# Kernel optimization log

Measured on AMD Instinct MI355X. Metric: run time of the kernel, lower is better.

The kernel has to match this reference:

```python
import jax, jax.numpy as jnp
import numpy as np

EPS = 1e-5  # GraphNorm eps


def setup_inputs() -> dict:
    key = jax.random.key(0)
    ks = jax.random.split(key, 8)
    B, N, D, L = 8, 2048, 128, 3
    return {
        "instance": jax.random.uniform(ks[0], (B, N, 2), jnp.float32),
        "Wn": jax.random.normal(ks[1], (D, 2), jnp.float32) * 0.5,
        "bn": jnp.zeros((D,), jnp.float32),
        "Wg": jax.random.normal(ks[2], (L, D, D), jnp.float32) / np.sqrt(D).astype(np.float32),
        "bg": jnp.zeros((L, D), jnp.float32),
        "gn_w": jnp.ones((D,), jnp.float32),
        "gn_b": jnp.zeros((D,), jnp.float32),
        "gn_a": jnp.ones((D,), jnp.float32),
    }


def reference(instance, Wn, bn, Wg, bg, gn_w, gn_b, gn_a):
    # instance: [B, N, 2] city coordinates. Graph is complete, so the PyG
    # edge-list GCN over all (i != j) pairs + self-loops is exactly a dense
    # symmetric-normalized adjacency matmul per graph.
    B, N, _ = instance.shape
    # pairwise Euclidean distances (cdist), safe sqrt to keep diagonal exact 0
    sq = jnp.sum(instance * instance, axis=-1)                      # [B, N]
    d2 = sq[:, :, None] + sq[:, None, :] - 2.0 * jnp.einsum(
        'bnd,bmd->bnm', instance, instance)                          # [B, N, N]
    pos = d2 > 0
    dist = jnp.where(pos, jnp.sqrt(jnp.where(pos, d2, 1.0)), 0.0)    # [B, N, N]
    # GCN edge weights = distances, self-loops added with weight 1.0
    A = dist + jnp.eye(N, dtype=dist.dtype)
    deg = jnp.sum(A, axis=-1)                                        # [B, N]
    dinv = jax.lax.rsqrt(deg)
    An = dinv[:, :, None] * A * dinv[:, None, :]                     # D^-1/2 A D^-1/2

    h = jnp.einsum('bne,de->bnd', instance, Wn) + bn                 # proj_node
    for l in range(Wg.shape[0]):
        # GCNConv: aggregate normalized messages of lin(x), then bias
        hw = jnp.einsum('bnm,bmd->bnd', An, jnp.einsum('bnd,ed->bne', h, Wg[l])) + bg[l]
        h = jnp.tanh(hw) + h                                         # activation + residual
        # GraphNorm (shared params across layers): per-graph, per-feature stats
        mean = jnp.mean(h, axis=1, keepdims=True)                    # [B, 1, D]
        sub = h - gn_a * mean
        var = jnp.mean(sub * sub, axis=1, keepdims=True)
        h = gn_w * sub * jax.lax.rsqrt(var + EPS) + gn_b
    return h  # [B, N, D] (unbatch+stack of equal-size graphs)
```

## Files before the change

kernel.cpp:

```cpp
#include <hip/hip_runtime.h>
#include <hip/hip_bf16.h>
#include <math.h>

#define BB 8
#define NN 2048
#define DD 128
#define LL 3
#define GN_EPS 1e-5f

typedef __attribute__((ext_vector_type(8))) short bf16x8;
typedef __attribute__((ext_vector_type(4))) float f32x4;
typedef __attribute__((ext_vector_type(8))) unsigned short u16x8;

#define FSQRT(x) __builtin_amdgcn_sqrtf(x)

#define GLL16(gp, lp) __builtin_amdgcn_global_load_lds( \
    (const __attribute__((address_space(1))) void*)(gp), \
    (__attribute__((address_space(3))) void*)(lp), 16, 0, 0)

#define WAIT_VM10 0x0F7A

__device__ __forceinline__ unsigned short f2bf(float f) {
    union { float f; unsigned u; } v; v.f = f;
    return (unsigned short)((v.u + 0x8000u) >> 16);
}

__device__ __forceinline__ float fast_tanh(float x) {
    float e = __expf(-2.0f * fabsf(x));
    float t = (1.0f - e) * __builtin_amdgcn_rcpf(1.0f + e);
    return copysignf(t, x);
}

__device__ __forceinline__ void stats_sc(float ps, float pq, float a, float w_,
                                         float b_, float& s, float& c) {
    const float inv_n = 1.0f / (float)NN;
    float mean = ps * inv_n;
    float msq  = pq * inv_n;
    float var  = msq - mean * mean * a * (2.0f - a);
    float rstd = rsqrtf(var + GN_EPS);
    s = w_ * rstd;
    c = b_ - s * (a * mean);
}


__global__ __launch_bounds__(256)
void prep_wg(const float* __restrict__ Wg, unsigned short* __restrict__ wgf)
{
    const int f = blockIdx.x * 256 + threadIdx.x;
    const int l  = f >> 14;
    const int r  = f & 16383;
    const int dp = r >> 7;
    const int e  = r & 127;
    const int dpt = dp >> 4, ll = dp & 15;
    const int kc  = e >> 5,  eo = e & 31;
    wgf[((((l * 8 + dpt) * 4 + kc) * 16 + ll) << 5) + eo] = f2bf(Wg[f]);
}

__global__ __launch_bounds__(256)
void gen_pack(const float* __restrict__ inst, const float* __restrict__ Wn,
              const float* __restrict__ bn, unsigned short* __restrict__ Ap,
              float* __restrict__ dinv, float* __restrict__ h,
              float* __restrict__ psum, float* __restrict__ psq)
{
    __shared__ float cs[NN * 2];
    __shared__ float part[4][16];
    const int b     = blockIdx.x & 7;
    const int ntile = blockIdx.x >> 3;
    const int n0    = ntile * 16;
    const int tid   = threadIdx.x;
    const int w     = tid >> 6;
    const int lane  = tid & 63;
    const int lq    = lane >> 4;
    const int ll    = lane & 15;

    const float* instb = inst + b * NN * 2;
    for (int i = tid; i < (NN * 2) / 4; i += 256)
        ((float4*)cs)[i] = ((const float4*)instb)[i];
    __syncthreads();

    const int n = n0 + ll;
    const float nx = cs[n * 2 + 0];
    const float ny = cs[n * 2 + 1];

    u16x8* apw = (u16x8*)Ap + (size_t)(b * 128 + ntile) * 64 * 64 + (w * 16) * 64 + lane;

    const int diagkcg = ntile >> 1;
    float rs = 0.f;
    for (int kc = 0; kc < 16; ++kc) {
        const int kcg = w * 16 + kc;
        const int mb  = kcg * 32 + lq * 8;
        const float* cp = &cs[mb * 2];
        float4 c01 = *(const float4*)(cp + 0);
        float4 c23 = *(const float4*)(cp + 4);
        float4 c45 = *(const float4*)(cp + 8);
        float4 c67 = *(const float4*)(cp + 12);
        float mxx[8] = { c01.x, c01.z, c23.x, c23.z, c45.x, c45.z, c67.x, c67.z };
        float myy[8] = { c01.y, c01.w, c23.y, c23.w, c45.y, c45.w, c67.y, c67.w };
        float dist[8];
        #pragma unroll
        for (int j = 0; j < 8; ++j) {
            float dx = nx - mxx[j];
            float dy = ny - myy[j];
            dist[j] = FSQRT(dx * dx + dy * dy);
        }
        if (kcg == diagkcg) {
            #pragma unroll
            for (int j = 0; j < 8; ++j)
                if (mb + j == n) dist[j] = 1.0f;
        }
        u16x8 pk;
        #pragma unroll
        for (int j = 0; j < 8; ++j) {
            pk[j] = f2bf(dist[j]);
            rs += dist[j];
        }
        apw[kc * 64] = pk;
    }

    rs += __shfl_xor(rs, 16);
    rs += __shfl_xor(rs, 32);
    if (lq == 0) part[w][ll] = rs;
    __syncthreads();
    if (tid < 16)
        dinv[b * NN + n0 + tid] = rsqrtf(part[0][tid] + part[1][tid] +
                                         part[2][tid] + part[3][tid]);

    {
        const int d  = tid & 127;
        const int r0 = tid >> 7;
        const float w0 = Wn[d * 2 + 0];
        const float w1 = Wn[d * 2 + 1];
        const float bv = bn[d];
        #pragma unroll
        for (int r = r0; r < 16; r += 2) {
            const float x0 = cs[(n0 + r) * 2 + 0];
            const float x1 = cs[(n0 + r) * 2 + 1];
            h[((size_t)b * NN + n0 + r) * DD + d] = fmaf(x0, w0, fmaf(x1, w1, bv));
        }
    }
    if (blockIdx.x == 0) {
        for (int i = tid; i < LL * BB * DD; i += 256) { psum[i] = 0.f; psq[i] = 0.f; }
    }
}

template <bool HP>
__global__ __launch_bounds__(256)
void lin_mfma(const float* __restrict__ h, const unsigned short* __restrict__ wgf_l,
              const float* __restrict__ dinv,
              const float* __restrict__ psumP, const float* __restrict__ psqP,
              const float* __restrict__ ga, const float* __restrict__ gw,
              const float* __restrict__ gb, unsigned short* __restrict__ tp)
{
    __shared__ float sL[DD], cL[DD];
    const int tid  = threadIdx.x;
    const int b    = blockIdx.x & 7;
    const int tile = blockIdx.x >> 3;
    const int row0 = b * NN + tile * 32;
    const int w    = tid >> 6;
    const int lane = tid & 63;
    const int lq   = lane >> 4;
    const int ll   = lane & 15;

    if (tid < DD) {
        float s = 1.0f, c = 0.0f;
        if (HP)
            stats_sc(psumP[b * DD + tid], psqP[b * DD + tid],
                     ga[tid], gw[tid], gb[tid], s, c);
        sL[tid] = s; cL[tid] = c;
    }
    __syncthreads();

    bf16x8 aw[2][4];
    #pragma unroll
    for (int mt = 0; mt < 2; ++mt) {
        const int dpt = 2 * w + mt;
        #pragma unroll
        for (int kc = 0; kc < 4; ++kc)
            aw[mt][kc] = *(const bf16x8*)&wgf_l[(((dpt * 4 + kc) * 16 + ll) << 5) + lq * 8];
    }

    bf16x8 bh[2][4];
    #pragma unroll
    for (int nt = 0; nt < 2; ++nt) {
        const float* hrow = h + (size_t)(row0 + nt * 16 + ll) * DD;
        #pragma unroll
        for (int kc = 0; kc < 4; ++kc) {
            float4 h0 = *(const float4*)&hrow[kc * 32 + lq * 8];
            float4 h1 = *(const float4*)&hrow[kc * 32 + lq * 8 + 4];
            const int e0 = kc * 32 + lq * 8;
            bf16x8 p;
            p[0] = (short)f2bf(fmaf(sL[e0 + 0], h0.x, cL[e0 + 0]));
            p[1] = (short)f2bf(fmaf(sL[e0 + 1], h0.y, cL[e0 + 1]));
            p[2] = (short)f2bf(fmaf(sL[e0 + 2], h0.z, cL[e0 + 2]));
            p[3] = (short)f2bf(fmaf(sL[e0 + 3], h0.w, cL[e0 + 3]));
            p[4] = (short)f2bf(fmaf(sL[e0 + 4], h1.x, cL[e0 + 4]));
            p[5] = (short)f2bf(fmaf(sL[e0 + 5], h1.y, cL[e0 + 5]));
            p[6] = (short)f2bf(fmaf(sL[e0 + 6], h1.z, cL[e0 + 6]));
            p[7] = (short)f2bf(fmaf(sL[e0 + 7], h1.w, cL[e0 + 7]));
            bh[nt][kc] = p;
        }
    }

    f32x4 acc[2][2];
    #pragma unroll
    for (int i = 0; i < 2; ++i)
        #pragma unroll
        for (int j = 0; j < 2; ++j) acc[i][j] = (f32x4)0.0f;

    #pragma unroll
    for (int kc = 0; kc < 4; ++kc)
        #pragma unroll
        for (int nt = 0; nt < 2; ++nt)
            #pragma unroll
            for (int mt = 0; mt < 2; ++mt)
                acc[nt][mt] = __builtin_amdgcn_mfma_f32_16x16x32_bf16(
                    bh[nt][kc], aw[mt][kc], acc[nt][mt], 0, 0, 0);

    #pragma unroll
    for (int nt = 0; nt < 2; ++nt) {
        const int mloc0 = nt * 16 + lq * 4;
        const int lq_a  = mloc0 >> 3;
        const int j0    = mloc0 & 7;
        float4 di4 = *(const float4*)&dinv[row0 + mloc0];
        #pragma unroll
        for (int mt = 0; mt < 2; ++mt) {
            const int dt = 2 * w + mt;
            ushort4 pk;
            pk.x = f2bf(acc[nt][mt][0] * di4.x);
            pk.y = f2bf(acc[nt][mt][1] * di4.y);
            pk.z = f2bf(acc[nt][mt][2] * di4.z);
            pk.w = f2bf(acc[nt][mt][3] * di4.w);
            *(ushort4*)&tp[((size_t)((b * 64 + tile) * 8 + dt) * 64 + lq_a * 16 + ll) * 8 + j0] = pk;
        }
    }
}

template <bool HP>
__global__ __launch_bounds__(256, 3)
void agg_mfma(const unsigned short* __restrict__ Ap, const unsigned short* __restrict__ tp,
              const float* __restrict__ dinv, const float* __restrict__ bg_l,
              const float* __restrict__ psumP, const float* __restrict__ psqP,
              const float* __restrict__ ga, const float* __restrict__ gw,
              const float* __restrict__ gb,
              float* __restrict__ h, float* __restrict__ psum, float* __restrict__ psq)
{
    __shared__ char Abuf[7][4096];
    const int b     = blockIdx.x & 7;
    const int ntile = blockIdx.x >> 3;
    const int n0    = ntile * 16;
    const int tid   = threadIdx.x;
    const int w     = tid >> 6;
    const int lane  = tid & 63;
    const int lq    = lane >> 4;
    const int ll    = lane & 15;

    const unsigned short* apsrc = Ap + ((size_t)(b * 128 + ntile) * 64) * 512 + lane * 8;
    const unsigned short* tpb   = tp + ((size_t)b * 64 * 8) * 512 + lane * 8;

    f32x4 acc[2];
    acc[0] = (f32x4)0.0f;
    acc[1] = (f32x4)0.0f;

    bf16x8 fb[3][2][4];

#define GLLA(c) GLL16(apsrc + (size_t)((((c) & 15) * 4 + w)) * 512, \
                      &Abuf[(c) % 7][w * 1024]);
#define LOADB(c) { \
        const int kb_ = ((c) & 15) * 4; \
        _Pragma("unroll") \
        for (int s_ = 0; s_ < 4; ++s_) { \
            fb[(c) % 3][0][s_] = *(const bf16x8*)(tpb + (size_t)((kb_ + s_) * 8 + 2 * w + 0) * 512); \
            fb[(c) % 3][1][s_] = *(const bf16x8*)(tpb + (size_t)((kb_ + s_) * 8 + 2 * w + 1) * 512); \
        } \
    }

    GLLA(0) GLLA(1) GLLA(2) GLLA(3)
    LOADB(0)
    GLLA(4)
    LOADB(1)
    GLLA(5)

    #pragma unroll
    for (int k = 0; k < 16; ++k) {
        __builtin_amdgcn_s_waitcnt(WAIT_VM10);
        __builtin_amdgcn_s_barrier();
        __builtin_amdgcn_sched_barrier(0);
        bf16x8 af[4];
        const char* lb = &Abuf[k % 7][0];
        #pragma unroll
        for (int s = 0; s < 4; ++s)
            af[s] = *(const bf16x8*)(lb + s * 1024 + lane * 16);
        LOADB(k + 2)
        GLLA(k + 6)
        __builtin_amdgcn_sched_barrier(0);
        #pragma unroll
        for (int s = 0; s < 4; ++s) {
            acc[0] = __builtin_amdgcn_mfma_f32_16x16x32_bf16(fb[k % 3][0][s], af[s], acc[0], 0, 0, 0);
            acc[1] = __builtin_amdgcn_mfma_f32_16x16x32_bf16(fb[k % 3][1][s], af[s], acc[1], 0, 0, 0);
        }
    }
#undef GLLA
#undef LOADB

    const int n  = n0 + ll;
    const float di = dinv[b * NN + n];
    #pragma unroll
    for (int dtl = 0; dtl < 2; ++dtl) {
        const int d0 = (2 * w + dtl) * 16 + lq * 4;
        float4 bg4 = *(const float4*)&bg_l[d0];
        float sres[4] = {1.f, 1.f, 1.f, 1.f}, cres[4] = {0.f, 0.f, 0.f, 0.f};
        if (HP) {
            float4 ps4 = *(const float4*)&psumP[b * DD + d0];
            float4 pq4 = *(const float4*)&psqP[b * DD + d0];
            float4 ga4 = *(const float4*)&ga[d0];
            float4 gw4 = *(const float4*)&gw[d0];
            float4 gb4 = *(const float4*)&gb[d0];
            stats_sc(ps4.x, pq4.x, ga4.x, gw4.x, gb4.x, sres[0], cres[0]);
            stats_sc(ps4.y, pq4.y, ga4.y, gw4.y, gb4.y, sres[1], cres[1]);
            stats_sc(ps4.z, pq4.z, ga4.z, gw4.z, gb4.z, sres[2], cres[2]);
            stats_sc(ps4.w, pq4.w, ga4.w, gw4.w, gb4.w, sres[3], cres[3]);
        }
        size_t idx = ((size_t)b * NN + n) * DD + d0;
        float4 hv = *(const float4*)&h[idx];
        float outv[4];
        #pragma unroll
        for (int r = 0; r < 4; ++r) {
            float pre = di * acc[dtl][r] + (&bg4.x)[r];
            outv[r] = fast_tanh(pre) + fmaf(sres[r], (&hv.x)[r], cres[r]);
        }
        float4 ov = { outv[0], outv[1], outv[2], outv[3] };
        *(float4*)&h[idx] = ov;

        float hs[4], hq[4];
        #pragma unroll
        for (int r = 0; r < 4; ++r) { hs[r] = outv[r]; hq[r] = outv[r] * outv[r]; }
        #pragma unroll
        for (int off = 1; off < 16; off <<= 1) {
            #pragma unroll
            for (int r = 0; r < 4; ++r) {
                hs[r] += __shfl_xor(hs[r], off);
                hq[r] += __shfl_xor(hq[r], off);
            }
        }
        if (ll == 0) {
            #pragma unroll
            for (int r = 0; r < 4; ++r) {
                atomicAdd(&psum[b * DD + d0 + r], hs[r]);
                atomicAdd(&psq[b * DD + d0 + r], hq[r]);
            }
        }
    }
}

__global__ __launch_bounds__(256)
void apply_kernel(const float* __restrict__ h,
                  const float* __restrict__ psum2, const float* __restrict__ psq2,
                  const float* __restrict__ ga, const float* __restrict__ gw,
                  const float* __restrict__ gb, float* __restrict__ dst)
{
    const int i4 = blockIdx.x * 256 + threadIdx.x;
    const int dg = (i4 & 31) * 4;
    const int b  = i4 >> 16;
    float4 hv = ((const float4*)h)[i4];
    float o[4];
    #pragma unroll
    for (int j = 0; j < 4; ++j) {
        const int d = dg + j;
        float s, c;
        stats_sc(psum2[b * DD + d], psq2[b * DD + d], ga[d], gw[d], gb[d], s, c);
        o[j] = fmaf(s, (&hv.x)[j], c);
    }
    float4 ov = { o[0], o[1], o[2], o[3] };
    ((float4*)dst)[i4] = ov;
}

extern "C" void kernel_launch(void* const* d_in, const int* in_sizes, int n_in,
                              void* d_out, int out_size, void* d_ws, size_t ws_size,
                              hipStream_t stream)
{
    const float* inst = (const float*)d_in[0];
    const float* Wn   = (const float*)d_in[1];
    const float* bn   = (const float*)d_in[2];
    const float* Wg   = (const float*)d_in[3];
    const float* bg   = (const float*)d_in[4];
    const float* gw   = (const float*)d_in[5];
    const float* gb   = (const float*)d_in[6];
    const float* ga   = (const float*)d_in[7];
    float* out = (float*)d_out;

    float* ws   = (float*)d_ws;
    float* dinv = ws;
    float* h    = dinv + BB * NN;
    float* psum = h + (size_t)BB * NN * DD;
    float* psq  = psum + LL * BB * DD;
    unsigned short* wgf = (unsigned short*)(psq + LL * BB * DD);
    unsigned short* tp  = wgf + LL * DD * DD;
    unsigned short* Ap  = tp + (size_t)BB * DD * NN;

    prep_wg<<<(LL * DD * DD) / 256, 256, 0, stream>>>(Wg, wgf);
    gen_pack<<<1024, 256, 0, stream>>>(inst, Wn, bn, Ap, dinv, h, psum, psq);

    for (int l = 0; l < LL; ++l) {
        const unsigned short* wgl = wgf + (size_t)l * DD * DD;
        const float* psP = psum + (size_t)(l - 1) * BB * DD;
        const float* pqP = psq  + (size_t)(l - 1) * BB * DD;
        float* psL = psum + (size_t)l * BB * DD;
        float* pqL = psq  + (size_t)l * BB * DD;
        if (l == 0) {
            lin_mfma<false><<<(BB * NN) / 32, 256, 0, stream>>>(
                h, wgl, dinv, nullptr, nullptr, ga, gw, gb, tp);
            agg_mfma<false><<<1024, 256, 0, stream>>>(
                Ap, tp, dinv, bg + l * DD, nullptr, nullptr, ga, gw, gb, h, psL, pqL);
        } else {
            lin_mfma<true><<<(BB * NN) / 32, 256, 0, stream>>>(
                h, wgl, dinv, psP, pqP, ga, gw, gb, tp);
            agg_mfma<true><<<1024, 256, 0, stream>>>(
                Ap, tp, dinv, bg + l * DD, psP, pqP, ga, gw, gb, h, psL, pqL);
        }
    }
    apply_kernel<<<(BB * NN * DD / 4) / 256, 256, 0, stream>>>(
        h, psum + 2 * BB * DD, psq + 2 * BB * DD, ga, gw, gb, out);
}
```

Baseline: 214.8 us.

## Fold first GCN linear into projection and double agg row tile

Precomputes Wg[0]·Wn and Wg[0]·bn so that gen_pack writes the first layer's scaled transformed features directly into tp. This removes the layer-0 lin_mfma launch. The aggregation kernel now processes 32 rows per block instead of 16, so each B-fragment load from tp is reused across two A tiles. That halves B traffic at the cost of more LDS per block, lower occupancy (launch bounds 2), and an adjusted waitcnt. The folded weights are computed serially by a single block in prep_wg.

```diff
diff --git a/kernel.cpp b/kernel.cpp
--- a/kernel.cpp
+++ b/kernel.cpp
@@ -18,7 +18,7 @@
     (const __attribute__((address_space(1))) void*)(gp), \
     (__attribute__((address_space(3))) void*)(lp), 16, 0, 0)
 
-#define WAIT_VM10 0x0F7A
+#define WAIT_VM12 0x0F7C
 
 __device__ __forceinline__ unsigned short f2bf(float f) {
     union { float f; unsigned u; } v; v.f = f;
@@ -44,7 +44,9 @@
 
 
 __global__ __launch_bounds__(256)
-void prep_wg(const float* __restrict__ Wg, unsigned short* __restrict__ wgf)
+void prep_wg(const float* __restrict__ Wg, const float* __restrict__ Wn,
+             const float* __restrict__ bn, unsigned short* __restrict__ wgf,
+             float* __restrict__ weff, float* __restrict__ beff)
 {
     const int f = blockIdx.x * 256 + threadIdx.x;
     const int l  = f >> 14;
@@ -54,12 +56,28 @@
     const int dpt = dp >> 4, ll = dp & 15;
     const int kc  = e >> 5,  eo = e & 31;
     wgf[((((l * 8 + dpt) * 4 + kc) * 16 + ll) << 5) + eo] = f2bf(Wg[f]);
+
+    if (blockIdx.x == 0 && threadIdx.x < 128) {
+        const int ee = threadIdx.x;
+        float a0 = 0.f, a1 = 0.f, cc = 0.f;
+        for (int d = 0; d < 128; ++d) {
+            const float wv = Wg[ee * 128 + d];
+            a0 = fmaf(wv, Wn[d * 2 + 0], a0);
+            a1 = fmaf(wv, Wn[d * 2 + 1], a1);
+            cc = fmaf(wv, bn[d], cc);
+        }
+        weff[ee * 2 + 0] = a0;
+        weff[ee * 2 + 1] = a1;
+        beff[ee] = cc;
+    }
 }
 
 __global__ __launch_bounds__(256)
 void gen_pack(const float* __restrict__ inst, const float* __restrict__ Wn,
-              const float* __restrict__ bn, unsigned short* __restrict__ Ap,
+              const float* __restrict__ bn, const float* __restrict__ weff,
+              const float* __restrict__ beff, unsigned short* __restrict__ Ap,
               float* __restrict__ dinv, float* __restrict__ h,
+              unsigned short* __restrict__ tp,
               float* __restrict__ psum, float* __restrict__ psq)
 {
     __shared__ float cs[NN * 2];
@@ -131,11 +149,25 @@
         const float w0 = Wn[d * 2 + 0];
         const float w1 = Wn[d * 2 + 1];
         const float bv = bn[d];
+        const float we0 = weff[d * 2 + 0];
+        const float we1 = weff[d * 2 + 1];
+        const float be  = beff[d];
+        const int kcg   = ntile >> 1;
+        const int mbase = (ntile & 1) * 16;
+        const int dt    = d >> 4;
+        const int lld   = d & 15;
+        unsigned short* tpd =
+            tp + (((size_t)(b * 64 + kcg) * 8 + dt) * 64 + lld) * 8;
         #pragma unroll
         for (int r = r0; r < 16; r += 2) {
             const float x0 = cs[(n0 + r) * 2 + 0];
             const float x1 = cs[(n0 + r) * 2 + 1];
             h[((size_t)b * NN + n0 + r) * DD + d] = fmaf(x0, w0, fmaf(x1, w1, bv));
+            const float dv = rsqrtf(part[0][r] + part[1][r] + part[2][r] + part[3][r]);
+            const int mloc = mbase + r;
+            const int lqa  = mloc >> 3;
+            const int j    = mloc & 7;
+            tpd[(size_t)lqa * 128 + j] = f2bf(dv * fmaf(x0, we0, fmaf(x1, we1, be)));
         }
     }
     if (blockIdx.x == 0) {
@@ -236,7 +268,7 @@
 }
 
 template <bool HP>
-__global__ __launch_bounds__(256, 3)
+__global__ __launch_bounds__(256, 2)
 void agg_mfma(const unsigned short* __restrict__ Ap, const unsigned short* __restrict__ tp,
               const float* __restrict__ dinv, const float* __restrict__ bg_l,
               const float* __restrict__ psumP, const float* __restrict__ psqP,
@@ -244,27 +276,31 @@
               const float* __restrict__ gb,
               float* __restrict__ h, float* __restrict__ psum, float* __restrict__ psq)
 {
-    __shared__ char Abuf[7][4096];
+    __shared__ char Abuf[7][8192];
     const int b     = blockIdx.x & 7;
-    const int ntile = blockIdx.x >> 3;
-    const int n0    = ntile * 16;
+    const int t2    = blockIdx.x >> 3;
+    const int n0    = t2 * 32;
     const int tid   = threadIdx.x;
     const int w     = tid >> 6;
     const int lane  = tid & 63;
     const int lq    = lane >> 4;
     const int ll    = lane & 15;
 
-    const unsigned short* apsrc = Ap + ((size_t)(b * 128 + ntile) * 64) * 512 + lane * 8;
+    const unsigned short* apsrc = Ap + ((size_t)(b * 128 + t2 * 2) * 64) * 512 + lane * 8;
     const unsigned short* tpb   = tp + ((size_t)b * 64 * 8) * 512 + lane * 8;
 
-    f32x4 acc[2];
-    acc[0] = (f32x4)0.0f;
-    acc[1] = (f32x4)0.0f;
+    f32x4 acc[2][2];
+    acc[0][0] = (f32x4)0.0f; acc[0][1] = (f32x4)0.0f;
+    acc[1][0] = (f32x4)0.0f; acc[1][1] = (f32x4)0.0f;
 
     bf16x8 fb[3][2][4];
 
-#define GLLA(c) GLL16(apsrc + (size_t)((((c) & 15) * 4 + w)) * 512, \
-                      &Abuf[(c) % 7][w * 1024]);
+#define GLLA(c) { \
+        GLL16(apsrc + (size_t)((((c) & 15) * 4 + w)) * 512, \
+              &Abuf[(c) % 7][w * 1024]); \
+        GLL16(apsrc + (size_t)((((c) & 15) * 4 + w)) * 512 + 32768, \
+              &Abuf[(c) % 7][4096 + w * 1024]); \
+    }
 #define LOADB(c) { \
         const int kb_ = ((c) & 15) * 4; \
         _Pragma("unroll") \
@@ -282,28 +318,33 @@
 
     #pragma unroll
     for (int k = 0; k < 16; ++k) {
-        __builtin_amdgcn_s_waitcnt(WAIT_VM10);
+        __builtin_amdgcn_s_waitcnt(WAIT_VM12);
         __builtin_amdgcn_s_barrier();
         __builtin_amdgcn_sched_barrier(0);
-        bf16x8 af[4];
+        bf16x8 af[2][4];
         const char* lb = &Abuf[k % 7][0];
         #pragma unroll
-        for (int s = 0; s < 4; ++s)
-            af[s] = *(const bf16x8*)(lb + s * 1024 + lane * 16);
+        for (int nt = 0; nt < 2; ++nt)
+            #pragma unroll
+            for (int s = 0; s < 4; ++s)
+                af[nt][s] = *(const bf16x8*)(lb + nt * 4096 + s * 1024 + lane * 16);
         LOADB(k + 2)
         GLLA(k + 6)
         __builtin_amdgcn_sched_barrier(0);
         #pragma unroll
         for (int s = 0; s < 4; ++s) {
-            acc[0] = __builtin_amdgcn_mfma_f32_16x16x32_bf16(fb[k % 3][0][s], af[s], acc[0], 0, 0, 0);
-            acc[1] = __builtin_amdgcn_mfma_f32_16x16x32_bf16(fb[k % 3][1][s], af[s], acc[1], 0, 0, 0);
+            #pragma unroll
+            for (int nt = 0; nt < 2; ++nt) {
+                acc[nt][0] = __builtin_amdgcn_mfma_f32_16x16x32_bf16(fb[k % 3][0][s], af[nt][s], acc[nt][0], 0, 0, 0);
+                acc[nt][1] = __builtin_amdgcn_mfma_f32_16x16x32_bf16(fb[k % 3][1][s], af[nt][s], acc[nt][1], 0, 0, 0);
+            }
         }
     }
 #undef GLLA
 #undef LOADB
 
-    const int n  = n0 + ll;
-    const float di = dinv[b * NN + n];
+    const float di0 = dinv[b * NN + n0 + ll];
+    const float di1 = dinv[b * NN + n0 + 16 + ll];
     #pragma unroll
     for (int dtl = 0; dtl < 2; ++dtl) {
         const int d0 = (2 * w + dtl) * 16 + lq * 4;
@@ -320,20 +361,25 @@
             stats_sc(ps4.z, pq4.z, ga4.z, gw4.z, gb4.z, sres[2], cres[2]);
             stats_sc(ps4.w, pq4.w, ga4.w, gw4.w, gb4.w, sres[3], cres[3]);
         }
-        size_t idx = ((size_t)b * NN + n) * DD + d0;
-        float4 hv = *(const float4*)&h[idx];
-        float outv[4];
-        #pragma unroll
-        for (int r = 0; r < 4; ++r) {
-            float pre = di * acc[dtl][r] + (&bg4.x)[r];
-            outv[r] = fast_tanh(pre) + fmaf(sres[r], (&hv.x)[r], cres[r]);
-        }
-        float4 ov = { outv[0], outv[1], outv[2], outv[3] };
-        *(float4*)&h[idx] = ov;
-
-        float hs[4], hq[4];
-        #pragma unroll
-        for (int r = 0; r < 4; ++r) { hs[r] = outv[r]; hq[r] = outv[r] * outv[r]; }
+        float hs[4] = {0.f, 0.f, 0.f, 0.f}, hq[4] = {0.f, 0.f, 0.f, 0.f};
+        #pragma unroll
+        for (int nt = 0; nt < 2; ++nt) {
+            const int n = n0 + nt * 16 + ll;
+            const float di = nt ? di1 : di0;
+            size_t idx = ((size_t)b * NN + n) * DD + d0;
+            float4 hv = *(const float4*)&h[idx];
+            float outv[4];
+            #pragma unroll
+            for (int r = 0; r < 4; ++r) {
+                float pre = di * acc[nt][dtl][r] + (&bg4.x)[r];
+                outv[r] = fast_tanh(pre) + fmaf(sres[r], (&hv.x)[r], cres[r]);
+                hs[r] += outv[r];
+                hq[r] += outv[r] * outv[r];
+            }
+            float4 ov = { outv[0], outv[1], outv[2], outv[3] };
+            *(float4*)&h[idx] = ov;
+        }
+
         #pragma unroll
         for (int off = 1; off < 16; off <<= 1) {
             #pragma unroll
@@ -393,30 +439,28 @@
     float* h    = dinv + BB * NN;
     float* psum = h + (size_t)BB * NN * DD;
     float* psq  = psum + LL * BB * DD;
-    unsigned short* wgf = (unsigned short*)(psq + LL * BB * DD);
+    float* weff = psq + LL * BB * DD;
+    float* beff = weff + 2 * DD;
+    unsigned short* wgf = (unsigned short*)(beff + DD);
     unsigned short* tp  = wgf + LL * DD * DD;
     unsigned short* Ap  = tp + (size_t)BB * DD * NN;
 
-    prep_wg<<<(LL * DD * DD) / 256, 256, 0, stream>>>(Wg, wgf);
-    gen_pack<<<1024, 256, 0, stream>>>(inst, Wn, bn, Ap, dinv, h, psum, psq);
-
-    for (int l = 0; l < LL; ++l) {
+    prep_wg<<<(LL * DD * DD) / 256, 256, 0, stream>>>(Wg, Wn, bn, wgf, weff, beff);
+    gen_pack<<<1024, 256, 0, stream>>>(inst, Wn, bn, weff, beff, Ap, dinv, h, tp, psum, psq);
+
+    agg_mfma<false><<<512, 256, 0, stream>>>(
+        Ap, tp, dinv, bg + 0 * DD, nullptr, nullptr, ga, gw, gb, h, psum, psq);
+
+    for (int l = 1; l < LL; ++l) {
         const unsigned short* wgl = wgf + (size_t)l * DD * DD;
         const float* psP = psum + (size_t)(l - 1) * BB * DD;
         const float* pqP = psq  + (size_t)(l - 1) * BB * DD;
         float* psL = psum + (size_t)l * BB * DD;
         float* pqL = psq  + (size_t)l * BB * DD;
-        if (l == 0) {
-            lin_mfma<false><<<(BB * NN) / 32, 256, 0, stream>>>(
-                h, wgl, dinv, nullptr, nullptr, ga, gw, gb, tp);
-            agg_mfma<false><<<1024, 256, 0, stream>>>(
-                Ap, tp, dinv, bg + l * DD, nullptr, nullptr, ga, gw, gb, h, psL, pqL);
-        } else {
-            lin_mfma<true><<<(BB * NN) / 32, 256, 0, stream>>>(
-                h, wgl, dinv, psP, pqP, ga, gw, gb, tp);
-            agg_mfma<true><<<1024, 256, 0, stream>>>(
-                Ap, tp, dinv, bg + l * DD, psP, pqP, ga, gw, gb, h, psL, pqL);
-        }
+        lin_mfma<true><<<(BB * NN) / 32, 256, 0, stream>>>(
+            h, wgl, dinv, psP, pqP, ga, gw, gb, tp);
+        agg_mfma<true><<<512, 256, 0, stream>>>(
+            Ap, tp, dinv, bg + l * DD, psP, pqP, ga, gw, gb, h, psL, pqL);
     }
     apply_kernel<<<(BB * NN * DD / 4) / 256, 256, 0, stream>>>(
         h, psum + 2 * BB * DD, psq + 2 * BB * DD, ga, gw, gb, out);
```

New measurement: 186.8 us. 13.0% less time.

## Recompute distance adjacency inside aggregation instead of storing packed bf16 matrix

Applied to the files above, without the earlier changes.

The aggregation kernel no longer reads a precomputed bf16 adjacency matrix from global memory. It now recomputes pairwise distances from coordinates staged in LDS, splits K across the four waves, and reduces the partial accumulators through shared memory. The first layer's linear transform is folded algebraically into gen_pack by composing Wg with the input projection, which removes one lin_mfma launch, and the Wg prep kernel is merged into gen_pack. This trades about 64 MB of adjacency traffic per layer for extra sqrt/ALU work and an LDS cross-wave reduction. The launch bound rises to 4 blocks per SM.

```diff
diff --git a/kernel.cpp b/kernel.cpp
--- a/kernel.cpp
+++ b/kernel.cpp
@@ -13,12 +13,6 @@
 typedef __attribute__((ext_vector_type(8))) unsigned short u16x8;
 
 #define FSQRT(x) __builtin_amdgcn_sqrtf(x)
-
-#define GLL16(gp, lp) __builtin_amdgcn_global_load_lds( \
-    (const __attribute__((address_space(1))) void*)(gp), \
-    (__attribute__((address_space(3))) void*)(lp), 16, 0, 0)
-
-#define WAIT_VM10 0x0F7A
 
 __device__ __forceinline__ unsigned short f2bf(float f) {
     union { float f; unsigned u; } v; v.f = f;
@@ -44,26 +38,16 @@
 
 
 __global__ __launch_bounds__(256)
-void prep_wg(const float* __restrict__ Wg, unsigned short* __restrict__ wgf)
-{
-    const int f = blockIdx.x * 256 + threadIdx.x;
-    const int l  = f >> 14;
-    const int r  = f & 16383;
-    const int dp = r >> 7;
-    const int e  = r & 127;
-    const int dpt = dp >> 4, ll = dp & 15;
-    const int kc  = e >> 5,  eo = e & 31;
-    wgf[((((l * 8 + dpt) * 4 + kc) * 16 + ll) << 5) + eo] = f2bf(Wg[f]);
-}
-
-__global__ __launch_bounds__(256)
 void gen_pack(const float* __restrict__ inst, const float* __restrict__ Wn,
-              const float* __restrict__ bn, unsigned short* __restrict__ Ap,
+              const float* __restrict__ bn, const float* __restrict__ Wg,
+              unsigned short* __restrict__ wgf,
               float* __restrict__ dinv, float* __restrict__ h,
+              unsigned short* __restrict__ tp,
               float* __restrict__ psum, float* __restrict__ psq)
 {
     __shared__ float cs[NN * 2];
     __shared__ float part[4][16];
+    __shared__ float weffL[2 * DD], beffL[DD];
     const int b     = blockIdx.x & 7;
     const int ntile = blockIdx.x >> 3;
     const int n0    = ntile * 16;
@@ -73,16 +57,39 @@
     const int lq    = lane >> 4;
     const int ll    = lane & 15;
 
+    if (blockIdx.x < 192) {
+        const int f = blockIdx.x * 256 + tid;
+        const int l  = f >> 14;
+        const int r  = f & 16383;
+        const int dp = r >> 7;
+        const int e  = r & 127;
+        const int dpt = dp >> 4, llp = dp & 15;
+        const int kc  = e >> 5,  eo = e & 31;
+        wgf[((((l * 8 + dpt) * 4 + kc) * 16 + llp) << 5) + eo] = f2bf(Wg[f]);
+    }
+
     const float* instb = inst + b * NN * 2;
     for (int i = tid; i < (NN * 2) / 4; i += 256)
         ((float4*)cs)[i] = ((const float4*)instb)[i];
+
+    if (tid < DD) {
+        const int ee = tid;
+        float a0 = 0.f, a1 = 0.f, cc = 0.f;
+        for (int d = 0; d < 128; ++d) {
+            const float wv = Wg[ee * 128 + d];
+            a0 = fmaf(wv, Wn[d * 2 + 0], a0);
+            a1 = fmaf(wv, Wn[d * 2 + 1], a1);
+            cc = fmaf(wv, bn[d], cc);
+        }
+        weffL[ee * 2 + 0] = a0;
+        weffL[ee * 2 + 1] = a1;
+        beffL[ee] = cc;
+    }
     __syncthreads();
 
     const int n = n0 + ll;
     const float nx = cs[n * 2 + 0];
     const float ny = cs[n * 2 + 1];
-
-    u16x8* apw = (u16x8*)Ap + (size_t)(b * 128 + ntile) * 64 * 64 + (w * 16) * 64 + lane;
 
     const int diagkcg = ntile >> 1;
     float rs = 0.f;
@@ -108,13 +115,8 @@
             for (int j = 0; j < 8; ++j)
                 if (mb + j == n) dist[j] = 1.0f;
         }
-        u16x8 pk;
-        #pragma unroll
-        for (int j = 0; j < 8; ++j) {
-            pk[j] = f2bf(dist[j]);
-            rs += dist[j];
-        }
-        apw[kc * 64] = pk;
+        #pragma unroll
+        for (int j = 0; j < 8; ++j) rs += dist[j];
     }
 
     rs += __shfl_xor(rs, 16);
@@ -131,11 +133,25 @@
         const float w0 = Wn[d * 2 + 0];
         const float w1 = Wn[d * 2 + 1];
         const float bv = bn[d];
+        const float we0 = weffL[d * 2 + 0];
+        const float we1 = weffL[d * 2 + 1];
+        const float be  = beffL[d];
+        const int kcg   = ntile >> 1;
+        const int mbase = (ntile & 1) * 16;
+        const int dt    = d >> 4;
+        const int lld   = d & 15;
+        unsigned short* tpd =
+            tp + (((size_t)(b * 64 + kcg) * 8 + dt) * 64 + lld) * 8;
         #pragma unroll
         for (int r = r0; r < 16; r += 2) {
             const float x0 = cs[(n0 + r) * 2 + 0];
             const float x1 = cs[(n0 + r) * 2 + 1];
             h[((size_t)b * NN + n0 + r) * DD + d] = fmaf(x0, w0, fmaf(x1, w1, bv));
+            const float dv = rsqrtf(part[0][r] + part[1][r] + part[2][r] + part[3][r]);
+            const int mloc = mbase + r;
+            const int lqa  = mloc >> 3;
+            const int j    = mloc & 7;
+            tpd[(size_t)lqa * 128 + j] = f2bf(dv * fmaf(x0, we0, fmaf(x1, we1, be)));
         }
     }
     if (blockIdx.x == 0) {
@@ -236,15 +252,16 @@
 }
 
 template <bool HP>
-__global__ __launch_bounds__(256, 3)
-void agg_mfma(const unsigned short* __restrict__ Ap, const unsigned short* __restrict__ tp,
+__global__ __launch_bounds__(256, 4)
+void agg_mfma(const float* __restrict__ inst, const unsigned short* __restrict__ tp,
               const float* __restrict__ dinv, const float* __restrict__ bg_l,
               const float* __restrict__ psumP, const float* __restrict__ psqP,
               const float* __restrict__ ga, const float* __restrict__ gw,
               const float* __restrict__ gb,
               float* __restrict__ h, float* __restrict__ psum, float* __restrict__ psq)
 {
-    __shared__ char Abuf[7][4096];
+    __shared__ __align__(16) char shm[32768];
+    float* cs = (float*)shm;
     const int b     = blockIdx.x & 7;
     const int ntile = blockIdx.x >> 3;
     const int n0    = ntile * 16;
@@ -254,56 +271,78 @@
     const int lq    = lane >> 4;
     const int ll    = lane & 15;
 
-    const unsigned short* apsrc = Ap + ((size_t)(b * 128 + ntile) * 64) * 512 + lane * 8;
-    const unsigned short* tpb   = tp + ((size_t)b * 64 * 8) * 512 + lane * 8;
-
-    f32x4 acc[2];
-    acc[0] = (f32x4)0.0f;
-    acc[1] = (f32x4)0.0f;
-
-    bf16x8 fb[3][2][4];
-
-#define GLLA(c) GLL16(apsrc + (size_t)((((c) & 15) * 4 + w)) * 512, \
-                      &Abuf[(c) % 7][w * 1024]);
-#define LOADB(c) { \
-        const int kb_ = ((c) & 15) * 4; \
-        _Pragma("unroll") \
-        for (int s_ = 0; s_ < 4; ++s_) { \
-            fb[(c) % 3][0][s_] = *(const bf16x8*)(tpb + (size_t)((kb_ + s_) * 8 + 2 * w + 0) * 512); \
-            fb[(c) % 3][1][s_] = *(const bf16x8*)(tpb + (size_t)((kb_ + s_) * 8 + 2 * w + 1) * 512); \
-        } \
-    }
-
-    GLLA(0) GLLA(1) GLLA(2) GLLA(3)
-    LOADB(0)
-    GLLA(4)
-    LOADB(1)
-    GLLA(5)
-
-    #pragma unroll
-    for (int k = 0; k < 16; ++k) {
-        __builtin_amdgcn_s_waitcnt(WAIT_VM10);
-        __builtin_amdgcn_s_barrier();
-        __builtin_amdgcn_sched_barrier(0);
-        bf16x8 af[4];
-        const char* lb = &Abuf[k % 7][0];
-        #pragma unroll
-        for (int s = 0; s < 4; ++s)
-            af[s] = *(const bf16x8*)(lb + s * 1024 + lane * 16);
-        LOADB(k + 2)
-        GLLA(k + 6)
-        __builtin_amdgcn_sched_barrier(0);
-        #pragma unroll
-        for (int s = 0; s < 4; ++s) {
-            acc[0] = __builtin_amdgcn_mfma_f32_16x16x32_bf16(fb[k % 3][0][s], af[s], acc[0], 0, 0, 0);
-            acc[1] = __builtin_amdgcn_mfma_f32_16x16x32_bf16(fb[k % 3][1][s], af[s], acc[1], 0, 0, 0);
-        }
-    }
-#undef GLLA
-#undef LOADB
-
-    const int n  = n0 + ll;
-    const float di = dinv[b * NN + n];
+    const float* instb = inst + b * NN * 2;
+    for (int i = tid; i < (NN * 2) / 4; i += 256)
+        ((float4*)cs)[i] = ((const float4*)instb)[i];
+
+    const unsigned short* tpb = tp + ((size_t)b * 64 * 8) * 512 + lane * 8;
+
+    f32x4 acc[8];
+    #pragma unroll
+    for (int dt = 0; dt < 8; ++dt) acc[dt] = (f32x4)0.0f;
+
+    bf16x8 fb[8];
+
+    __syncthreads();
+
+    const int   nr = n0 + ll;
+    const float nx = cs[nr * 2 + 0], ny = cs[nr * 2 + 1];
+    const int diagk = ntile >> 1;
+    const int kcg0  = w * 16;
+
+    #pragma unroll
+    for (int kc = 0; kc < 16; ++kc) {
+        const int kcg_ = kcg0 + kc;
+        #pragma unroll
+        for (int dt = 0; dt < 8; ++dt)
+            fb[dt] = *(const bf16x8*)(tpb + (size_t)(kcg_ * 8 + dt) * 512);
+        const int mb_ = kcg_ * 32 + lq * 8;
+        const float* cp_ = &cs[mb_ * 2];
+        float4 c01 = *(const float4*)(cp_ + 0);
+        float4 c23 = *(const float4*)(cp_ + 4);
+        float4 c45 = *(const float4*)(cp_ + 8);
+        float4 c67 = *(const float4*)(cp_ + 12);
+        float dv[8];
+        {
+            float mxx[8] = { c01.x, c01.z, c23.x, c23.z, c45.x, c45.z, c67.x, c67.z };
+            float myy[8] = { c01.y, c01.w, c23.y, c23.w, c45.y, c45.w, c67.y, c67.w };
+            #pragma unroll
+            for (int j = 0; j < 8; ++j) {
+                float dx = nx - mxx[j], dy = ny - myy[j];
+                dv[j] = FSQRT(dx * dx + dy * dy);
+            }
+        }
+        if (kcg_ == diagk) {
+            #pragma unroll
+            for (int j = 0; j < 8; ++j)
+                if (mb_ + j == nr) dv[j] = 1.0f;
+        }
+        bf16x8 af;
+        #pragma unroll
+        for (int j = 0; j < 8; ++j) af[j] = (short)f2bf(dv[j]);
+        #pragma unroll
+        for (int dt = 0; dt < 8; ++dt)
+            acc[dt] = __builtin_amdgcn_mfma_f32_16x16x32_bf16(fb[dt], af, acc[dt], 0, 0, 0);
+    }
+
+    __syncthreads();
+    #pragma unroll
+    for (int dt = 0; dt < 8; ++dt)
+        *(f32x4*)(shm + ((dt * 4 + w) * 1024) + lane * 16) = acc[dt];
+    __syncthreads();
+
+    f32x4 accs[2];
+    #pragma unroll
+    for (int dtl = 0; dtl < 2; ++dtl) {
+        const int dt = 2 * w + dtl;
+        f32x4 r0 = *(const f32x4*)(shm + ((dt * 4 + 0) * 1024) + lane * 16);
+        f32x4 r1 = *(const f32x4*)(shm + ((dt * 4 + 1) * 1024) + lane * 16);
+        f32x4 r2 = *(const f32x4*)(shm + ((dt * 4 + 2) * 1024) + lane * 16);
+        f32x4 r3 = *(const f32x4*)(shm + ((dt * 4 + 3) * 1024) + lane * 16);
+        accs[dtl] = ((r0 + r1) + r2) + r3;
+    }
+
+    const float di = dinv[b * NN + nr];
     #pragma unroll
     for (int dtl = 0; dtl < 2; ++dtl) {
         const int d0 = (2 * w + dtl) * 16 + lq * 4;
@@ -320,20 +359,20 @@
             stats_sc(ps4.z, pq4.z, ga4.z, gw4.z, gb4.z, sres[2], cres[2]);
             stats_sc(ps4.w, pq4.w, ga4.w, gw4.w, gb4.w, sres[3], cres[3]);
         }
-        size_t idx = ((size_t)b * NN + n) * DD + d0;
+        size_t idx = ((size_t)b * NN + nr) * DD + d0;
         float4 hv = *(const float4*)&h[idx];
         float outv[4];
+        float hs[4], hq[4];
         #pragma unroll
         for (int r = 0; r < 4; ++r) {
-            float pre = di * acc[dtl][r] + (&bg4.x)[r];
+            float pre = di * accs[dtl][r] + (&bg4.x)[r];
             outv[r] = fast_tanh(pre) + fmaf(sres[r], (&hv.x)[r], cres[r]);
+            hs[r] = outv[r];
+            hq[r] = outv[r] * outv[r];
         }
         float4 ov = { outv[0], outv[1], outv[2], outv[3] };
         *(float4*)&h[idx] = ov;
 
-        float hs[4], hq[4];
-        #pragma unroll
-        for (int r = 0; r < 4; ++r) { hs[r] = outv[r]; hq[r] = outv[r] * outv[r]; }
         #pragma unroll
         for (int off = 1; off < 16; off <<= 1) {
             #pragma unroll
@@ -395,28 +434,22 @@
     float* psq  = psum + LL * BB * DD;
     unsigned short* wgf = (unsigned short*)(psq + LL * BB * DD);
     unsigned short* tp  = wgf + LL * DD * DD;
-    unsigned short* Ap  = tp + (size_t)BB * DD * NN;
-
-    prep_wg<<<(LL * DD * DD) / 256, 256, 0, stream>>>(Wg, wgf);
-    gen_pack<<<1024, 256, 0, stream>>>(inst, Wn, bn, Ap, dinv, h, psum, psq);
-
-    for (int l = 0; l < LL; ++l) {
+
+    gen_pack<<<1024, 256, 0, stream>>>(inst, Wn, bn, Wg, wgf, dinv, h, tp, psum, psq);
+
+    agg_mfma<false><<<1024, 256, 0, stream>>>(
+        inst, tp, dinv, bg + 0 * DD, nullptr, nullptr, ga, gw, gb, h, psum, psq);
+
+    for (int l = 1; l < LL; ++l) {
         const unsigned short* wgl = wgf + (size_t)l * DD * DD;
         const float* psP = psum + (size_t)(l - 1) * BB * DD;
         const float* pqP = psq  + (size_t)(l - 1) * BB * DD;
         float* psL = psum + (size_t)l * BB * DD;
         float* pqL = psq  + (size_t)l * BB * DD;
-        if (l == 0) {
-            lin_mfma<false><<<(BB * NN) / 32, 256, 0, stream>>>(
-                h, wgl, dinv, nullptr, nullptr, ga, gw, gb, tp);
-            agg_mfma<false><<<1024, 256, 0, stream>>>(
-                Ap, tp, dinv, bg + l * DD, nullptr, nullptr, ga, gw, gb, h, psL, pqL);
-        } else {
-            lin_mfma<true><<<(BB * NN) / 32, 256, 0, stream>>>(
-                h, wgl, dinv, psP, pqP, ga, gw, gb, tp);
-            agg_mfma<true><<<1024, 256, 0, stream>>>(
-                Ap, tp, dinv, bg + l * DD, psP, pqP, ga, gw, gb, h, psL, pqL);
-        }
+        lin_mfma<true><<<(BB * NN) / 32, 256, 0, stream>>>(
+            h, wgl, dinv, psP, pqP, ga, gw, gb, tp);
+        agg_mfma<true><<<1024, 256, 0, stream>>>(
+            inst, tp, dinv, bg + l * DD, psP, pqP, ga, gw, gb, h, psL, pqL);
     }
     apply_kernel<<<(BB * NN * DD / 4) / 256, 256, 0, stream>>>(
         h, psum + 2 * BB * DD, psq + 2 * BB * DD, ga, gw, gb, out);
```

New measurement: 196.8 us. -8.4%, faster.
